# Performance work log

Measured on AMD Instinct MI355X. Metric: run time of the kernel, lower is better.

Reference implementation:

```python
import math
import jax, jax.numpy as jnp
import numpy as np

B, L, D = 8, 2048, 1024
NEG_INF = 1e9  # config.INF stand-in; large finite value keeps fully-masked rows NaN-free


def setup_inputs() -> dict:
    key = jax.random.key(0)
    k1, k2, k3, k4, k5, k6 = jax.random.split(key, 6)
    s = 1.0 / math.sqrt(D)
    return {
        "input_seq": jax.random.normal(k1, (B, L, D), dtype=jnp.float32),
        "input_lens": jax.random.randint(k2, (B,), 1, L + 1, dtype=jnp.int64),
        "output_seq": jax.random.normal(k3, (B, L, D), dtype=jnp.float32),
        "Wk": jax.random.normal(k4, (D, D), dtype=jnp.float32) * s,
        "Wv": jax.random.normal(k5, (D, D), dtype=jnp.float32) * s,
        "Wq": jax.random.normal(k6, (D, D), dtype=jnp.float32) * s,
    }


def reference(input_seq, input_lens, output_seq, Wk, Wv, Wq):
    # Linear(embed_dim, embed_dim, bias=False): y = x @ W^T
    k = jnp.einsum('bld,ed->ble', input_seq, Wk)   # [B, L, D]
    v = jnp.einsum('bld,ed->ble', input_seq, Wv)   # [B, L, D]
    q = jnp.einsum('bld,ed->ble', output_seq, Wq)  # [B, L, D]

    scores = jnp.einsum('bqd,bkd->bqk', q, k) / math.sqrt(D)  # [B, Lq, Lk]

    # Faithful to the torch code (apply_mask=True): mask [B, L] is unsqueezed
    # on the LAST dim -> [B, L, 1], so it broadcasts over the KEY axis and
    # effectively masks query rows with index >= input_lens.
    valid = jnp.arange(L)[None, :] < input_lens[:, None]      # [B, L]
    scores = jnp.where(valid[:, :, None], scores, -NEG_INF)

    attn = jax.nn.softmax(scores, axis=-1)                    # [B, Lq, Lk]
    # dropout is identity in eval mode (deterministic reference)
    context = jnp.einsum('bqk,bkd->bqd', attn, v)             # [B, Lq, D]
    return context, attn
```

## Files before the change

### kernel.cpp

```cpp
#include <hip/hip_runtime.h>
#include <hip/hip_bf16.h>

#define B_ 8
#define L_ 2048
#define D_ 1024
#define CTX_ELEMS (B_ * L_ * D_)

typedef __bf16 bf16x8 __attribute__((ext_vector_type(8)));
typedef float f32x4 __attribute__((ext_vector_type(4)));
typedef unsigned short u16x8 __attribute__((ext_vector_type(8)));
typedef unsigned short u16x4 __attribute__((ext_vector_type(4)));

typedef __attribute__((address_space(1))) void GV;
typedef __attribute__((address_space(3))) void LV;
#define GLL16(g, l) __builtin_amdgcn_global_load_lds((GV*)(g), (LV*)(l), 16, 0, 0)

__device__ __forceinline__ unsigned short f2bf(float f) {
    union { float f; unsigned u; } c; c.f = f;
    unsigned u = c.u;
    u += 0x7fffu + ((u >> 16) & 1u);
    return (unsigned short)(u >> 16);
}

__global__ __launch_bounds__(256) void cvt_kernel(
    const float* __restrict__ x, const float* __restrict__ y,
    const float* __restrict__ Wk, const float* __restrict__ Wv,
    const float* __restrict__ Wq,
    unsigned short* __restrict__ xb, unsigned short* __restrict__ yb,
    unsigned short* __restrict__ wkb, unsigned short* __restrict__ wvb,
    unsigned short* __restrict__ wqb)
{
    const float* src; unsigned short* dst; int n4;
    switch (blockIdx.y) {
        case 0:  src = x;  dst = xb;  n4 = CTX_ELEMS / 4; break;
        case 1:  src = y;  dst = yb;  n4 = CTX_ELEMS / 4; break;
        case 2:  src = Wk; dst = wkb; n4 = D_ * D_ / 4;   break;
        case 3:  src = Wv; dst = wvb; n4 = D_ * D_ / 4;   break;
        default: src = Wq; dst = wqb; n4 = D_ * D_ / 4;   break;
    }
    const int stride = gridDim.x * 256;
    for (int i = blockIdx.x * 256 + threadIdx.x; i < n4; i += stride) {
        float4 f = ((const float4*)src)[i];
        u16x4 o = { f2bf(f.x), f2bf(f.y), f2bf(f.z), f2bf(f.w) };
        ((u16x4*)dst)[i] = o;
    }
}

#define GEMM_VARS                                              \
    const int tid = threadIdx.x;                               \
    const int wave = tid >> 6, lane = tid & 63;                \
    const int wr = wave >> 1, wc = wave & 1;                   \
    const int lrow = lane & 15, quad = lane >> 4;              \
    const int gr = lane >> 2, gc = (lane & 3) * 8;

#define GEMM_KLOOP(Ag, lda, Bg, ldb, K)                                        \
    for (int k0 = 0; k0 < (K); k0 += 32) {                                     \
        __syncthreads();                                                       \
        _Pragma("unroll")                                                      \
        for (int r = 0; r < 2; r++) {                                          \
            const int seg = wave * 2 + r;                                      \
            GLL16((Ag) + (size_t)(m0 + seg * 16 + gr) * (lda) + k0 + gc,       \
                  sA + seg * 512);                                             \
            GLL16((Bg) + (size_t)(n0 + seg * 16 + gr) * (ldb) + k0 + gc,       \
                  sB + seg * 512);                                             \
        }                                                                      \
        __syncthreads();                                                       \
        bf16x8 av[4], bv[4];                                                   \
        _Pragma("unroll")                                                      \
        for (int i = 0; i < 4; i++)                                            \
            av[i] = *(const bf16x8*)&sA[(wr * 64 + i * 16 + lrow) * 32 + quad * 8]; \
        _Pragma("unroll")                                                      \
        for (int j = 0; j < 4; j++)                                            \
            bv[j] = *(const bf16x8*)&sB[(wc * 64 + j * 16 + lrow) * 32 + quad * 8]; \
        _Pragma("unroll")                                                      \
        for (int i = 0; i < 4; i++)                                            \
            _Pragma("unroll")                                                  \
            for (int j = 0; j < 4; j++)                                        \
                acc[i][j] = __builtin_amdgcn_mfma_f32_16x16x32_bf16(           \
                    av[i], bv[j], acc[i][j], 0, 0, 0);                         \
    }

__global__ __launch_bounds__(256) void proj_kernel(
    const unsigned short* __restrict__ xb, const unsigned short* __restrict__ yb,
    const unsigned short* __restrict__ wkb, const unsigned short* __restrict__ wvb,
    const unsigned short* __restrict__ wqb,
    unsigned short* __restrict__ kb, unsigned short* __restrict__ qb,
    unsigned short* __restrict__ vtb)
{
    __shared__ unsigned short smem[8192];
    unsigned short* sA = smem;
    unsigned short* sB = smem + 4096;

    const int z = blockIdx.z;
    const int lin = blockIdx.x;
    const int sq = lin >> 4, w = lin & 15;
    const int big = (sq & 31) * 4 + (w & 3);
    const int sml = (sq >> 5) * 4 + (w >> 2);
    int m0, n0;
    const unsigned short *Ag, *Bg;
    if (z == 0)      { Ag = xb;  Bg = wkb; m0 = big * 128; n0 = sml * 128; }
    else if (z == 1) { Ag = wvb; Bg = xb;  m0 = sml * 128; n0 = big * 128; }
    else             { Ag = yb;  Bg = wqb; m0 = big * 128; n0 = sml * 128; }

    GEMM_VARS

    f32x4 acc[4][4];
#pragma unroll
    for (int i = 0; i < 4; i++)
#pragma unroll
        for (int j = 0; j < 4; j++) acc[i][j] = (f32x4){0.f, 0.f, 0.f, 0.f};

    GEMM_KLOOP(Ag, D_, Bg, D_, D_)

    unsigned short* base; size_t ostride;
    if (z == 1) {
        base = vtb + (size_t)(n0 >> 11) * D_ * L_ + (size_t)m0 * L_ + (n0 & 2047);
        ostride = L_;
    } else {
        base = ((z == 0) ? kb : qb) + (size_t)m0 * D_ + n0;
        ostride = D_;
    }

#pragma unroll
    for (int h = 0; h < 2; h++) {
        __syncthreads();
        if (wr == h) {
#pragma unroll
            for (int i = 0; i < 4; i++)
#pragma unroll
                for (int j = 0; j < 4; j++)
#pragma unroll
                    for (int r = 0; r < 4; r++)
                        smem[(i * 16 + quad * 4 + r) * 128 + wc * 64 + j * 16 + lrow]
                            = f2bf(acc[i][j][r]);
        }
        __syncthreads();
#pragma unroll
        for (int c = 0; c < 4; c++) {
            const int idx = c * 256 + tid;
            const int rr  = idx >> 4;
            const int c8  = (idx & 15) * 8;
            *(u16x8*)(base + (size_t)(h * 64 + rr) * ostride + c8)
                = *(const u16x8*)&smem[rr * 128 + c8];
        }
    }
}

__global__ __launch_bounds__(256) void scores_kernel(
    const unsigned short* __restrict__ qb, const unsigned short* __restrict__ kb,
    float* __restrict__ attn)
{
    __shared__ unsigned short smem[8192];
    unsigned short* sA = smem;
    unsigned short* sB = smem + 4096;

    const int bz = blockIdx.z;
    const unsigned short* Ag = qb + (size_t)bz * L_ * D_;
    const unsigned short* Bg = kb + (size_t)bz * L_ * D_;
    float* out = attn + (size_t)bz * L_ * L_;

    const int lin = blockIdx.x;
    const int sq = lin >> 4, w = lin & 15;
    const int m0 = ((sq & 3) * 4 + (w & 3)) * 128;
    const int n0 = ((sq >> 2) * 4 + (w >> 2)) * 128;

    GEMM_VARS

    f32x4 acc[4][4];
#pragma unroll
    for (int i = 0; i < 4; i++)
#pragma unroll
        for (int j = 0; j < 4; j++) acc[i][j] = (f32x4){0.f, 0.f, 0.f, 0.f};

    GEMM_KLOOP(Ag, D_, Bg, D_, D_)

#pragma unroll
    for (int i = 0; i < 4; i++) {
        const int m = m0 + wr * 64 + i * 16 + quad * 4;
#pragma unroll
        for (int j = 0; j < 4; j++) {
            const int n = n0 + wc * 64 + j * 16 + lrow;
#pragma unroll
            for (int r = 0; r < 4; r++)
                out[(size_t)(m + r) * L_ + n] = acc[i][j][r] * 0.03125f;
        }
    }
}

__global__ __launch_bounds__(256) void softmax_kernel(
    float* __restrict__ attn, const int* __restrict__ lens,
    unsigned short* __restrict__ attn_bf)
{
    const int r  = blockIdx.x;
    const int b  = r >> 11;
    const int qi = r & 2047;
    float4* rowp = (float4*)(attn + (size_t)r * L_);
    u16x4*  rowb = (u16x4*)(attn_bf + (size_t)r * L_);
    const int tid = threadIdx.x;

    if (qi >= lens[b]) {
        const float u = 1.0f / 2048.0f;
        const unsigned short us = f2bf(u);
        const float4 uf = {u, u, u, u};
        const u16x4 ub = {us, us, us, us};
        rowp[tid] = uf; rowp[tid + 256] = uf;
        rowb[tid] = ub; rowb[tid + 256] = ub;
        return;
    }

    float4 v0 = rowp[tid], v1 = rowp[tid + 256];

    float m = fmaxf(fmaxf(fmaxf(v0.x, v0.y), fmaxf(v0.z, v0.w)),
                    fmaxf(fmaxf(v1.x, v1.y), fmaxf(v1.z, v1.w)));
#pragma unroll
    for (int off = 32; off > 0; off >>= 1) m = fmaxf(m, __shfl_xor(m, off, 64));

    __shared__ float redm[4];
    __shared__ float reds[4];
    const int wave = tid >> 6, lane = tid & 63;
    if (lane == 0) redm[wave] = m;
    __syncthreads();
    m = fmaxf(fmaxf(redm[0], redm[1]), fmaxf(redm[2], redm[3]));

    v0.x = __expf(v0.x - m); v0.y = __expf(v0.y - m);
    v0.z = __expf(v0.z - m); v0.w = __expf(v0.w - m);
    v1.x = __expf(v1.x - m); v1.y = __expf(v1.y - m);
    v1.z = __expf(v1.z - m); v1.w = __expf(v1.w - m);
    float s = (v0.x + v0.y) + (v0.z + v0.w) + (v1.x + v1.y) + (v1.z + v1.w);
#pragma unroll
    for (int off = 32; off > 0; off >>= 1) s += __shfl_xor(s, off, 64);
    if (lane == 0) reds[wave] = s;
    __syncthreads();
    s = reds[0] + reds[1] + reds[2] + reds[3];

    const float inv = 1.0f / s;
    v0.x *= inv; v0.y *= inv; v0.z *= inv; v0.w *= inv;
    v1.x *= inv; v1.y *= inv; v1.z *= inv; v1.w *= inv;
    rowp[tid] = v0; rowp[tid + 256] = v1;
    u16x4 b0 = { f2bf(v0.x), f2bf(v0.y), f2bf(v0.z), f2bf(v0.w) };
    u16x4 b1 = { f2bf(v1.x), f2bf(v1.y), f2bf(v1.z), f2bf(v1.w) };
    rowb[tid] = b0; rowb[tid + 256] = b1;
}

__global__ __launch_bounds__(256) void context_kernel(
    const unsigned short* __restrict__ attn_bf, const unsigned short* __restrict__ vtb,
    float* __restrict__ ctx)
{
    __shared__ unsigned short smem[8192];
    unsigned short* sA = smem;
    unsigned short* sB = smem + 4096;

    const int bz = blockIdx.z;
    const unsigned short* Ag = attn_bf + (size_t)bz * L_ * L_;
    const unsigned short* Bg = vtb + (size_t)bz * D_ * L_;
    float* out = ctx + (size_t)bz * L_ * D_;

    const int lin = blockIdx.x;
    const int sq = lin >> 4, w = lin & 15;
    const int m0 = ((sq & 3) * 4 + (w & 3)) * 128;
    const int n0 = ((sq >> 2) * 4 + (w >> 2)) * 128;

    GEMM_VARS

    f32x4 acc[4][4];
#pragma unroll
    for (int i = 0; i < 4; i++)
#pragma unroll
        for (int j = 0; j < 4; j++) acc[i][j] = (f32x4){0.f, 0.f, 0.f, 0.f};

    GEMM_KLOOP(Ag, L_, Bg, L_, L_)

#pragma unroll
    for (int i = 0; i < 4; i++) {
        const int m = m0 + wr * 64 + i * 16 + quad * 4;
#pragma unroll
        for (int j = 0; j < 4; j++) {
            const int n = n0 + wc * 64 + j * 16 + lrow;
#pragma unroll
            for (int r = 0; r < 4; r++)
                out[(size_t)(m + r) * D_ + n] = acc[i][j][r];
        }
    }
}

extern "C" void kernel_launch(void* const* d_in, const int* in_sizes, int n_in,
                              void* d_out, int out_size, void* d_ws, size_t ws_size,
                              hipStream_t stream) {
    const float* x    = (const float*)d_in[0];
    const int*   lens = (const int*)d_in[1];
    const float* y    = (const float*)d_in[2];
    const float* Wk   = (const float*)d_in[3];
    const float* Wv   = (const float*)d_in[4];
    const float* Wq   = (const float*)d_in[5];

    float* ctx  = (float*)d_out;
    float* attn = (float*)d_out + CTX_ELEMS;

    unsigned short* kb      = (unsigned short*)d_ws;
    unsigned short* qb      = kb + CTX_ELEMS;
    unsigned short* vtb     = qb + CTX_ELEMS;
    unsigned short* attn_bf = (unsigned short*)d_ws;

    unsigned short* xb  = (unsigned short*)attn;
    unsigned short* yb  = xb + CTX_ELEMS;
    unsigned short* wkb = yb + CTX_ELEMS;
    unsigned short* wvb = wkb + D_ * D_;
    unsigned short* wqb = wvb + D_ * D_;

    cvt_kernel<<<dim3(2048, 5), 256, 0, stream>>>(x, y, Wk, Wv, Wq,
                                                  xb, yb, wkb, wvb, wqb);
    proj_kernel<<<dim3(1024, 1, 3), 256, 0, stream>>>(xb, yb, wkb, wvb, wqb,
                                                      kb, qb, vtb);
    scores_kernel<<<dim3(256, 1, B_), 256, 0, stream>>>(qb, kb, attn);
    softmax_kernel<<<dim3(B_ * L_), 256, 0, stream>>>(attn, lens, attn_bf);
    context_kernel<<<dim3(128, 1, B_), 256, 0, stream>>>(attn_bf, vtb, ctx);
}
```

Baseline: 647.7 us.

## Replace GEMM core with 256x256 tiles, 4-stage LDS pipeline and swizzled layout

Rewrites the shared GEMM main loop used by the projection, scores and context kernels. Tiles grow from 128x128 to 256x256 with 8 waves per block, and a 4-deep global_load_lds ring buffer in 128KB of dynamic LDS overlaps loads with MFMA. LDS columns are XOR-swizzled to avoid bank conflicts, and each k-step is split into two MFMA halves with s_setprio and barriers. This targets the latency-bound single-buffered loop of the old kernels, at the cost of fewer blocks (grids shrink) and hand-managed waitcnt counts that must match the exact load schedule.

```diff
diff --git a/kernel.cpp b/kernel.cpp
--- a/kernel.cpp
+++ b/kernel.cpp
@@ -46,71 +46,97 @@
     }
 }
 
-#define GEMM_VARS                                              \
-    const int tid = threadIdx.x;                               \
-    const int wave = tid >> 6, lane = tid & 63;                \
-    const int wr = wave >> 1, wc = wave & 1;                   \
-    const int lrow = lane & 15, quad = lane >> 4;              \
-    const int gr = lane >> 2, gc = (lane & 3) * 8;
-
-#define GEMM_KLOOP(Ag, lda, Bg, ldb, K)                                        \
-    for (int k0 = 0; k0 < (K); k0 += 32) {                                     \
-        __syncthreads();                                                       \
-        _Pragma("unroll")                                                      \
-        for (int r = 0; r < 2; r++) {                                          \
-            const int seg = wave * 2 + r;                                      \
-            GLL16((Ag) + (size_t)(m0 + seg * 16 + gr) * (lda) + k0 + gc,       \
-                  sA + seg * 512);                                             \
-            GLL16((Bg) + (size_t)(n0 + seg * 16 + gr) * (ldb) + k0 + gc,       \
-                  sB + seg * 512);                                             \
-        }                                                                      \
-        __syncthreads();                                                       \
-        bf16x8 av[4], bv[4];                                                   \
-        _Pragma("unroll")                                                      \
-        for (int i = 0; i < 4; i++)                                            \
-            av[i] = *(const bf16x8*)&sA[(wr * 64 + i * 16 + lrow) * 32 + quad * 8]; \
-        _Pragma("unroll")                                                      \
-        for (int j = 0; j < 4; j++)                                            \
-            bv[j] = *(const bf16x8*)&sB[(wc * 64 + j * 16 + lrow) * 32 + quad * 8]; \
-        _Pragma("unroll")                                                      \
-        for (int i = 0; i < 4; i++)                                            \
-            _Pragma("unroll")                                                  \
-            for (int j = 0; j < 4; j++)                                        \
-                acc[i][j] = __builtin_amdgcn_mfma_f32_16x16x32_bf16(           \
-                    av[i], bv[j], acc[i][j], 0, 0, 0);                         \
-    }
-
-__global__ __launch_bounds__(256) void proj_kernel(
+#define BARx()  __builtin_amdgcn_s_barrier()
+#define LGKM0() do { asm volatile("s_waitcnt lgkmcnt(0)" ::: "memory"); \
+                     __builtin_amdgcn_sched_barrier(0); } while (0)
+#define PRIO(p) __builtin_amdgcn_s_setprio(p)
+
+#define G256_VARS \
+    const int tid = threadIdx.x; \
+    const int wave = tid >> 6, lane = tid & 63; \
+    const int wr = wave >> 2, wc = wave & 3; \
+    const int lrow = lane & 15, quad = lane >> 4; \
+    const int srow = lane >> 2; \
+    const int colsw = ((lane & 3) ^ ((lane >> 3) & 3)) << 3; \
+    const int colgrp = (quad ^ ((lrow >> 1) & 3)) << 4; \
+    const int pA = (wr * 128 + lrow) * 64 + colgrp; \
+    const int pB = (wc * 64 + lrow) * 64 + colgrp;
+
+#define STAGE_A(s, kk) do { \
+    GLL16(srcA0 + (kk), smem + (s) * 16384 + wave * 1024); \
+    GLL16(srcA1 + (kk), smem + (s) * 16384 + wave * 1024 + 512); } while (0)
+#define STAGE_B(s, kk) do { \
+    GLL16(srcB0 + (kk), smem + (s) * 16384 + 8192 + wave * 1024); \
+    GLL16(srcB1 + (kk), smem + (s) * 16384 + 8192 + wave * 1024 + 512); } while (0)
+
+#define G256_KLOOP(Ag, lda, Bg, ldb, NT) \
+    const unsigned short* srcA0 = (Ag) + (size_t)(m0 + wave * 32 + srow) * (lda) + colsw; \
+    const unsigned short* srcA1 = srcA0 + 16 * (size_t)(lda); \
+    const unsigned short* srcB0 = (Bg) + (size_t)(n0 + wave * 32 + srow) * (ldb) + colsw; \
+    const unsigned short* srcB1 = srcB0 + 16 * (size_t)(ldb); \
+    f32x4 acc[8][4]; \
+    _Pragma("unroll") \
+    for (int i = 0; i < 8; i++) \
+        _Pragma("unroll") \
+        for (int j = 0; j < 4; j++) acc[i][j] = (f32x4){0.f, 0.f, 0.f, 0.f}; \
+    _Pragma("unroll") \
+    for (int s = 0; s < 3; s++) { STAGE_A(s, s * 32); STAGE_B(s, s * 32); } \
+    asm volatile("s_waitcnt vmcnt(8)" ::: "memory"); \
+    BARx(); \
+    for (int t = 0; t < (NT); ++t) { \
+        const char* As = (const char*)smem + (t & 3) * 32768; \
+        const char* Bs = As + 16384; \
+        const int ss = (t + 3) & 3, kk = (t + 3) * 32; \
+        bf16x8 av[8], bv[4]; \
+        _Pragma("unroll") \
+        for (int i = 0; i < 4; i++) av[i] = *(const bf16x8*)(As + pA + i * 1024); \
+        _Pragma("unroll") \
+        for (int j = 0; j < 4; j++) bv[j] = *(const bf16x8*)(Bs + pB + j * 1024); \
+        if (t < (NT) - 3) STAGE_A(ss, kk); \
+        BARx(); LGKM0(); \
+        PRIO(1); \
+        _Pragma("unroll") \
+        for (int i = 0; i < 4; i++) \
+            _Pragma("unroll") \
+            for (int j = 0; j < 4; j++) \
+                acc[i][j] = __builtin_amdgcn_mfma_f32_16x16x32_bf16(av[i], bv[j], acc[i][j], 0, 0, 0); \
+        PRIO(0); \
+        BARx(); \
+        _Pragma("unroll") \
+        for (int i = 4; i < 8; i++) av[i] = *(const bf16x8*)(As + pA + i * 1024); \
+        if (t < (NT) - 3) STAGE_B(ss, kk); \
+        BARx(); LGKM0(); \
+        PRIO(1); \
+        _Pragma("unroll") \
+        for (int i = 4; i < 8; i++) \
+            _Pragma("unroll") \
+            for (int j = 0; j < 4; j++) \
+                acc[i][j] = __builtin_amdgcn_mfma_f32_16x16x32_bf16(av[i], bv[j], acc[i][j], 0, 0, 0); \
+        PRIO(0); \
+        if (t < (NT) - 3)      { asm volatile("s_waitcnt vmcnt(8)" ::: "memory"); } \
+        else if (t == (NT) - 3) { asm volatile("s_waitcnt vmcnt(4)" ::: "memory"); } \
+        else if (t == (NT) - 2) { asm volatile("s_waitcnt vmcnt(0)" ::: "memory"); } \
+        if (t < (NT) - 1) BARx(); \
+    }
+
+__global__ __launch_bounds__(512, 2) void proj_kernel(
     const unsigned short* __restrict__ xb, const unsigned short* __restrict__ yb,
     const unsigned short* __restrict__ wkb, const unsigned short* __restrict__ wvb,
     const unsigned short* __restrict__ wqb,
     unsigned short* __restrict__ kb, unsigned short* __restrict__ qb,
     unsigned short* __restrict__ vtb)
 {
-    __shared__ unsigned short smem[8192];
-    unsigned short* sA = smem;
-    unsigned short* sB = smem + 4096;
-
+    extern __shared__ unsigned short smem[];
     const int z = blockIdx.z;
     const int lin = blockIdx.x;
-    const int sq = lin >> 4, w = lin & 15;
-    const int big = (sq & 31) * 4 + (w & 3);
-    const int sml = (sq >> 5) * 4 + (w >> 2);
     int m0, n0;
     const unsigned short *Ag, *Bg;
-    if (z == 0)      { Ag = xb;  Bg = wkb; m0 = big * 128; n0 = sml * 128; }
-    else if (z == 1) { Ag = wvb; Bg = xb;  m0 = sml * 128; n0 = big * 128; }
-    else             { Ag = yb;  Bg = wqb; m0 = big * 128; n0 = sml * 128; }
-
-    GEMM_VARS
-
-    f32x4 acc[4][4];
-#pragma unroll
-    for (int i = 0; i < 4; i++)
-#pragma unroll
-        for (int j = 0; j < 4; j++) acc[i][j] = (f32x4){0.f, 0.f, 0.f, 0.f};
-
-    GEMM_KLOOP(Ag, D_, Bg, D_, D_)
+    if (z == 0)      { Ag = xb;  Bg = wkb; m0 = (lin >> 2) * 256; n0 = (lin & 3) * 256; }
+    else if (z == 1) { Ag = wvb; Bg = xb;  m0 = (lin & 3) * 256;  n0 = (lin >> 2) * 256; }
+    else             { Ag = yb;  Bg = wqb; m0 = (lin >> 2) * 256; n0 = (lin & 3) * 256; }
+
+    G256_VARS
+    G256_KLOOP(Ag, D_, Bg, D_, 32)
 
     unsigned short* base; size_t ostride;
     if (z == 1) {
@@ -121,62 +147,47 @@
         ostride = D_;
     }
 
-#pragma unroll
-    for (int h = 0; h < 2; h++) {
-        __syncthreads();
-        if (wr == h) {
-#pragma unroll
-            for (int i = 0; i < 4; i++)
-#pragma unroll
-                for (int j = 0; j < 4; j++)
-#pragma unroll
-                    for (int r = 0; r < 4; r++)
-                        smem[(i * 16 + quad * 4 + r) * 128 + wc * 64 + j * 16 + lrow]
-                            = f2bf(acc[i][j][r]);
-        }
-        __syncthreads();
-#pragma unroll
-        for (int c = 0; c < 4; c++) {
-            const int idx = c * 256 + tid;
-            const int rr  = idx >> 4;
-            const int c8  = (idx & 15) * 8;
-            *(u16x8*)(base + (size_t)(h * 64 + rr) * ostride + c8)
-                = *(const u16x8*)&smem[rr * 128 + c8];
-        }
-    }
-}
-
-__global__ __launch_bounds__(256) void scores_kernel(
+    __syncthreads();
+#pragma unroll
+    for (int i = 0; i < 8; i++)
+#pragma unroll
+        for (int j = 0; j < 4; j++)
+#pragma unroll
+            for (int r = 0; r < 4; r++) {
+                const int row = wr * 128 + i * 16 + quad * 4 + r;
+                const int col = wc * 64 + j * 16 + lrow;
+                const int off = (row * 512 + col * 2) ^ ((row & 12) << 3);
+                *(unsigned short*)((char*)smem + off) = f2bf(acc[i][j][r]);
+            }
+    __syncthreads();
+#pragma unroll
+    for (int c = 0; c < 16; c++) {
+        const int idx = c * 512 + tid;
+        const int rr = idx >> 5, cc = idx & 31;
+        const int off = (rr * 512 + cc * 16) ^ ((rr & 12) << 3);
+        *(u16x8*)(base + (size_t)rr * ostride + cc * 8)
+            = *(const u16x8*)((const char*)smem + off);
+    }
+}
+
+__global__ __launch_bounds__(512, 2) void scores_kernel(
     const unsigned short* __restrict__ qb, const unsigned short* __restrict__ kb,
     float* __restrict__ attn)
 {
-    __shared__ unsigned short smem[8192];
-    unsigned short* sA = smem;
-    unsigned short* sB = smem + 4096;
-
+    extern __shared__ unsigned short smem[];
     const int bz = blockIdx.z;
     const unsigned short* Ag = qb + (size_t)bz * L_ * D_;
     const unsigned short* Bg = kb + (size_t)bz * L_ * D_;
     float* out = attn + (size_t)bz * L_ * L_;
-
     const int lin = blockIdx.x;
-    const int sq = lin >> 4, w = lin & 15;
-    const int m0 = ((sq & 3) * 4 + (w & 3)) * 128;
-    const int n0 = ((sq >> 2) * 4 + (w >> 2)) * 128;
-
-    GEMM_VARS
-
-    f32x4 acc[4][4];
-#pragma unroll
-    for (int i = 0; i < 4; i++)
-#pragma unroll
-        for (int j = 0; j < 4; j++) acc[i][j] = (f32x4){0.f, 0.f, 0.f, 0.f};
-
-    GEMM_KLOOP(Ag, D_, Bg, D_, D_)
-
-#pragma unroll
-    for (int i = 0; i < 4; i++) {
-        const int m = m0 + wr * 64 + i * 16 + quad * 4;
+    const int m0 = (lin >> 3) * 256, n0 = (lin & 7) * 256;
+
+    G256_VARS
+    G256_KLOOP(Ag, D_, Bg, D_, 32)
+
+#pragma unroll
+    for (int i = 0; i < 8; i++) {
+        const int m = m0 + wr * 128 + i * 16 + quad * 4;
 #pragma unroll
         for (int j = 0; j < 4; j++) {
             const int n = n0 + wc * 64 + j * 16 + lrow;
@@ -242,37 +253,24 @@
     rowb[tid] = b0; rowb[tid + 256] = b1;
 }
 
-__global__ __launch_bounds__(256) void context_kernel(
+__global__ __launch_bounds__(512, 2) void context_kernel(
     const unsigned short* __restrict__ attn_bf, const unsigned short* __restrict__ vtb,
     float* __restrict__ ctx)
 {
-    __shared__ unsigned short smem[8192];
-    unsigned short* sA = smem;
-    unsigned short* sB = smem + 4096;
-
+    extern __shared__ unsigned short smem[];
     const int bz = blockIdx.z;
     const unsigned short* Ag = attn_bf + (size_t)bz * L_ * L_;
     const unsigned short* Bg = vtb + (size_t)bz * D_ * L_;
     float* out = ctx + (size_t)bz * L_ * D_;
-
     const int lin = blockIdx.x;
-    const int sq = lin >> 4, w = lin & 15;
-    const int m0 = ((sq & 3) * 4 + (w & 3)) * 128;
-    const int n0 = ((sq >> 2) * 4 + (w >> 2)) * 128;
-
-    GEMM_VARS
-
-    f32x4 acc[4][4];
-#pragma unroll
-    for (int i = 0; i < 4; i++)
-#pragma unroll
-        for (int j = 0; j < 4; j++) acc[i][j] = (f32x4){0.f, 0.f, 0.f, 0.f};
-
-    GEMM_KLOOP(Ag, L_, Bg, L_, L_)
-
-#pragma unroll
-    for (int i = 0; i < 4; i++) {
-        const int m = m0 + wr * 64 + i * 16 + quad * 4;
+    const int m0 = (lin >> 2) * 256, n0 = (lin & 3) * 256;
+
+    G256_VARS
+    G256_KLOOP(Ag, L_, Bg, L_, 64)
+
+#pragma unroll
+    for (int i = 0; i < 8; i++) {
+        const int m = m0 + wr * 128 + i * 16 + quad * 4;
 #pragma unroll
         for (int j = 0; j < 4; j++) {
             const int n = n0 + wc * 64 + j * 16 + lrow;
@@ -307,11 +305,18 @@
     unsigned short* wvb = wkb + D_ * D_;
     unsigned short* wqb = wvb + D_ * D_;
 
+    (void)hipFuncSetAttribute((const void*)proj_kernel,
+                              hipFuncAttributeMaxDynamicSharedMemorySize, 131072);
+    (void)hipFuncSetAttribute((const void*)scores_kernel,
+                              hipFuncAttributeMaxDynamicSharedMemorySize, 131072);
+    (void)hipFuncSetAttribute((const void*)context_kernel,
+                              hipFuncAttributeMaxDynamicSharedMemorySize, 131072);
+
     cvt_kernel<<<dim3(2048, 5), 256, 0, stream>>>(x, y, Wk, Wv, Wq,
                                                   xb, yb, wkb, wvb, wqb);
-    proj_kernel<<<dim3(1024, 1, 3), 256, 0, stream>>>(xb, yb, wkb, wvb, wqb,
-                                                      kb, qb, vtb);
-    scores_kernel<<<dim3(256, 1, B_), 256, 0, stream>>>(qb, kb, attn);
+    proj_kernel<<<dim3(256, 1, 3), 512, 131072, stream>>>(xb, yb, wkb, wvb, wqb,
+                                                          kb, qb, vtb);
+    scores_kernel<<<dim3(64, 1, 8), 512, 131072, stream>>>(qb, kb, attn);
     softmax_kernel<<<dim3(B_ * L_), 256, 0, stream>>>(attn, lens, attn_bf);
-    context_kernel<<<dim3(128, 1, B_), 256, 0, stream>>>(attn_bf, vtb, ctx);
-}
+    context_kernel<<<dim3(32, 1, 8), 512, 131072, stream>>>(attn_bf, vtb, ctx);
+}
```

After: 583.9 us. -9.8%, faster.
